# Kernel tuning notes

Measured on AMD Instinct MI355X. Metric: run time of the kernel, lower is better.

## Reference

```python
import jax, jax.numpy as jnp
import numpy as np

Q_STEPS, Q_TOKENS = 16, 64
KV_STEPS, KV_TOKENS = 64, 64
WINDOW = 2
TOPK = 32
DIM = 512
BATCH = 8
NUM_CONTEXTS = 2


def build_local_mask(q_steps, q_tokens, kv_steps, kv_tokens, window):
    # centers: nearest kv step for each query step
    centers = np.round(np.linspace(0, kv_steps - 1, q_steps)).astype(np.int64)
    steps = np.arange(kv_steps)
    allowed = np.abs(steps[None, :] - centers[:, None]) <= window  # [q_steps, kv_steps]
    allowed = np.repeat(np.repeat(allowed, q_tokens, axis=0), kv_tokens, axis=1)
    return jnp.where(jnp.asarray(allowed), 0.0, -jnp.inf).astype(jnp.float32)


MASK = build_local_mask(Q_STEPS, Q_TOKENS, KV_STEPS, KV_TOKENS, WINDOW)


def setup_inputs() -> dict:
    key = jax.random.key(0)
    ks = jax.random.split(key, 12)
    s = 1.0 / np.sqrt(DIM)
    return {
        "query": jax.random.normal(ks[0], (BATCH, Q_STEPS, Q_TOKENS, DIM), jnp.float32),
        "source": jax.random.normal(ks[1], (BATCH, KV_STEPS, KV_TOKENS, DIM), jnp.float32),
        "ctx1": jax.random.normal(ks[2], (BATCH, DIM), jnp.float32),
        "ctx2": jax.random.normal(ks[3], (BATCH, DIM), jnp.float32),
        "Wq": jax.random.normal(ks[4], (DIM, DIM), jnp.float32) * s,
        "bq": jnp.zeros((DIM,), jnp.float32),
        "Wk": jax.random.normal(ks[5], (DIM, DIM), jnp.float32) * s,
        "bk": jnp.zeros((DIM,), jnp.float32),
        "Wv": jax.random.normal(ks[6], (DIM, DIM), jnp.float32) * s,
        "bv": jnp.zeros((DIM,), jnp.float32),
        "Wo": jax.random.normal(ks[7], (DIM, DIM), jnp.float32) * s,
        "bo": jnp.zeros((DIM,), jnp.float32),
        "Wc": jax.random.normal(ks[8], (NUM_CONTEXTS * DIM, 2 * DIM), jnp.float32) * s,
        "bc": jnp.zeros((2 * DIM,), jnp.float32),
    }


def reference(query, source, ctx1, ctx2, Wq, bq, Wk, bk, Wv, bv, Wo, bo, Wc, bc):
    B = query.shape[0]
    # CrossScaleCondition: fuse contexts -> per-batch FiLM params gamma, beta [B, dim]
    fused = jnp.concatenate([ctx1, ctx2], axis=-1)          # [B, num_contexts*dim]
    gb = fused @ Wc + bc                                     # [B, 2*dim]
    gamma, beta = jnp.split(gb, 2, axis=-1)

    q_flat = query.reshape(B, Q_STEPS * Q_TOKENS, DIM)       # [B, Lq, d]
    src_flat = source.reshape(B, KV_STEPS * KV_TOKENS, DIM)  # [B, Lkv, d]

    q_mod = q_flat * (1.0 + gamma[:, None, :]) + beta[:, None, :]
    q = q_mod @ Wq + bq
    k = src_flat @ Wk + bk
    v = src_flat @ Wv + bv

    scores = jnp.einsum('bqd,bkd->bqk', q, k) / jnp.sqrt(jnp.float32(DIM))
    scores = scores + MASK[None]                             # local window mask

    topk_scores, topk_idx = jax.lax.top_k(scores, TOPK)      # [B, Lq, k]
    selected_v = jax.vmap(lambda vb, ib: vb[ib])(v, topk_idx)  # [B, Lq, k, d]

    attn = jax.nn.softmax(topk_scores, axis=-1)
    out = jnp.einsum('bqk,bqkd->bqd', attn, selected_v)
    out = out @ Wo + bo
    return out.reshape(B, Q_STEPS, Q_TOKENS, DIM)
```

## Files before the change

kernel.cpp:

```cpp
#include <hip/hip_runtime.h>

#define NWIN 320
#define SCORE_SCALE 0.04419417382415922f

__constant__ int CENTERS[16] = {0,4,8,13,17,21,25,29,34,38,42,46,50,55,59,63};

typedef __attribute__((ext_vector_type(8))) short v8s;
typedef __attribute__((ext_vector_type(4))) float v4f;

__device__ __forceinline__ float bflo(unsigned u) { return __uint_as_float(u << 16); }
__device__ __forceinline__ float bfhi(unsigned u) { return __uint_as_float(u & 0xffff0000u); }
__device__ __forceinline__ float bf2f(unsigned short h) { return __uint_as_float(((unsigned)h) << 16); }
__device__ __forceinline__ unsigned short f2bf(float x) {
  unsigned u = __float_as_uint(x);
  unsigned r = 0x7fffu + ((u >> 16) & 1u);
  return (unsigned short)((u + r) >> 16);
}

__device__ __forceinline__ int t64_off(int r, int k) {
  return ((r & 31) << 7) + (((((r >> 5) << 2) | (k >> 3)) ^ (r & 7)) << 4) + ((k & 7) << 1);
}
__device__ __forceinline__ int frag_off(int r, int g) {
  return ((r & 31) << 7) + (((((r >> 5) << 2) | g) ^ (r & 7)) << 4);
}

__device__ __forceinline__ void gload_lds16(const void* g, void* l) {
  __builtin_amdgcn_global_load_lds((const __attribute__((address_space(1))) unsigned int*)g,
                                   (__attribute__((address_space(3))) unsigned int*)l, 16, 0, 0);
}

__device__ __forceinline__ void cvt8pair(float4 a, float4 b, uint4& hi4, uint4& lo4) {
  float v[8] = {a.x, a.y, a.z, a.w, b.x, b.y, b.z, b.w};
  unsigned short h[8], l[8];
  #pragma unroll
  for (int e = 0; e < 8; ++e) {
    h[e] = f2bf(v[e]);
    l[e] = f2bf(v[e] - bf2f(h[e]));
  }
  hi4.x = (unsigned)h[0] | ((unsigned)h[1] << 16);
  hi4.y = (unsigned)h[2] | ((unsigned)h[3] << 16);
  hi4.z = (unsigned)h[4] | ((unsigned)h[5] << 16);
  hi4.w = (unsigned)h[6] | ((unsigned)h[7] << 16);
  lo4.x = (unsigned)l[0] | ((unsigned)l[1] << 16);
  lo4.y = (unsigned)l[2] | ((unsigned)l[3] << 16);
  lo4.z = (unsigned)l[4] | ((unsigned)l[5] << 16);
  lo4.w = (unsigned)l[6] | ((unsigned)l[7] << 16);
}

__device__ __forceinline__ uint4 cvt8hi(float4 a, float4 b) {
  uint4 r;
  r.x = (unsigned)f2bf(a.x) | ((unsigned)f2bf(a.y) << 16);
  r.y = (unsigned)f2bf(a.z) | ((unsigned)f2bf(a.w) << 16);
  r.z = (unsigned)f2bf(b.x) | ((unsigned)f2bf(b.y) << 16);
  r.w = (unsigned)f2bf(b.z) | ((unsigned)f2bf(b.w) << 16);
  return r;
}

__device__ __forceinline__ uint2 cvt4(float4 a) {
  uint2 r;
  r.x = (unsigned)f2bf(a.x) | ((unsigned)f2bf(a.y) << 16);
  r.y = (unsigned)f2bf(a.z) | ((unsigned)f2bf(a.w) << 16);
  return r;
}

__global__ void film_part(const float* __restrict__ ctx1, const float* __restrict__ ctx2,
                          const float* __restrict__ Wc, float* __restrict__ part)
{
  const int b = blockIdx.y, sl = blockIdx.x, j = threadIdx.x;
  const int i0 = sl * 128;
  float acc = 0.f;
  #pragma unroll 4
  for (int t = 0; t < 128; ++t) {
    const int i = i0 + t;
    const float f = (i < 512) ? ctx1[b * 512 + i] : ctx2[b * 512 + i - 512];
    acc = fmaf(f, Wc[(size_t)i * 1024 + j], acc);
  }
  part[(b * 8 + sl) * 1024 + j] = acc;
}

__global__ void film_reduce(const float* __restrict__ part, const float* __restrict__ bc,
                            float* __restrict__ gb)
{
  const int b = blockIdx.x, j = threadIdx.x;
  float acc = bc[j];
  #pragma unroll
  for (int sl = 0; sl < 8; ++sl) acc += part[(b * 8 + sl) * 1024 + j];
  gb[b * 1024 + j] = acc;
}

__global__ void u_kernel(const float* __restrict__ Wk, const float* __restrict__ bq,
                         float* __restrict__ u)
{
  const int d = blockIdx.x, lane = threadIdx.x;
  float4 a0 = *(const float4*)&Wk[(size_t)d * 512 + lane * 8];
  float4 a1 = *(const float4*)&Wk[(size_t)d * 512 + lane * 8 + 4];
  float4 c0 = *(const float4*)&bq[lane * 8];
  float4 c1 = *(const float4*)&bq[lane * 8 + 4];
  float s = a0.x*c0.x + a0.y*c0.y + a0.z*c0.z + a0.w*c0.w
          + a1.x*c1.x + a1.y*c1.y + a1.z*c1.z + a1.w*c1.w;
  #pragma unroll
  for (int off = 32; off > 0; off >>= 1) s += __shfl_xor(s, off, 64);
  if (lane == 0) u[d] = s * SCORE_SCALE;
}

__global__ __launch_bounds__(256) void wsplit_kernel(
    const float* __restrict__ Wq, const float* __restrict__ Wk,
    unsigned short* __restrict__ Wqh, unsigned short* __restrict__ Wql,
    unsigned short* __restrict__ Wkh, unsigned short* __restrict__ Wkl)
{
  const int b = blockIdx.x;
  const int mat = b >> 7;
  const float* Wsrc = mat ? Wk : Wq;
  unsigned short* Wh = mat ? Wkh : Wqh;
  unsigned short* Wl = mat ? Wkl : Wql;
  const size_t e0 = (((size_t)(b & 127) * 256) + threadIdx.x) * 8;
  float4 x0 = *(const float4*)&Wsrc[e0];
  float4 x1 = *(const float4*)&Wsrc[e0 + 4];
  uint4 h4, l4;
  cvt8pair(x0, x1, h4, l4);
  *(uint4*)&Wh[e0] = h4;
  *(uint4*)&Wl[e0] = l4;
}

__global__ __launch_bounds__(256) void gmat_mfma(
    const unsigned short* __restrict__ Wqh, const unsigned short* __restrict__ Wql,
    const unsigned short* __restrict__ Wkh, const unsigned short* __restrict__ Wkl,
    unsigned short* __restrict__ Gt)
{
  const int tid  = threadIdx.x;
  const int lane = tid & 63, l15 = lane & 15, g = lane >> 4;
  const int wave = tid >> 6;
  const int t  = ((int)blockIdx.x << 2) | wave;
  const int ti = t >> 5, tj = t & 31;
  const int ib = ti << 4, jb = tj << 4;
  const size_t arow = (size_t)(ib + l15) * 512 + (g << 3);
  const size_t brow = (size_t)(jb + l15) * 512 + (g << 3);

  v4f acc = (v4f){0.f, 0.f, 0.f, 0.f};
  #pragma unroll 4
  for (int kk = 0; kk < 16; ++kk) {
    const int kd = kk * 32;
    const v8s ah = *(const v8s*)&Wqh[arow + kd];
    const v8s al = *(const v8s*)&Wql[arow + kd];
    const v8s bh = *(const v8s*)&Wkh[brow + kd];
    const v8s bl = *(const v8s*)&Wkl[brow + kd];
    acc = __builtin_amdgcn_mfma_f32_16x16x32_bf16(ah, bh, acc, 0, 0, 0);
    acc = __builtin_amdgcn_mfma_f32_16x16x32_bf16(al, bh, acc, 0, 0, 0);
    acc = __builtin_amdgcn_mfma_f32_16x16x32_bf16(ah, bl, acc, 0, 0, 0);
  }

  #pragma unroll
  for (int k = 0; k < 4; ++k) {
    const int gi = ib + (g << 2) + k;
    const int gj = jb + l15;
    const float v = acc[k] * SCORE_SCALE;
    const unsigned short hi = f2bf(v);
    const unsigned short lo = f2bf(v - bf2f(hi));
    const int toff = t64_off(gj & 63, gi & 31);
    *(unsigned short*)((char*)Gt + ((size_t)((gi >> 5) * 8 + (gj >> 6)) << 12) + toff) = hi;
    *(unsigned short*)((char*)Gt + ((size_t)(((gi >> 5) + 16) * 8 + (gj >> 6)) << 12) + toff) = lo;
  }
}

__global__ __launch_bounds__(256) void wconv_kernel(
    const float* __restrict__ Wv, const float* __restrict__ Wo,
    unsigned short* __restrict__ Wvt, unsigned short* __restrict__ Wot)
{
  __shared__ char img[32768];
  const int ktile = blockIdx.x;
  const int mat   = blockIdx.y;
  const float* W = mat ? Wo : Wv;
  unsigned short* Dt = mat ? Wot : Wvt;
  const int tid = threadIdx.x;
  const int k  = tid >> 3;
  const int nt = tid & 7;
  #pragma unroll
  for (int e4 = 0; e4 < 16; ++e4) {
    float4 w = *(const float4*)&W[(size_t)(ktile * 32 + k) * 512 + nt * 64 + e4 * 4];
    float vv[4] = {w.x, w.y, w.z, w.w};
    #pragma unroll
    for (int c = 0; c < 4; ++c) {
      const int n = e4 * 4 + c;
      *(unsigned short*)(img + nt * 4096 + t64_off(n, k)) = f2bf(vv[c]);
    }
  }
  __syncthreads();
  const uint4* src = (const uint4*)img;
  uint4* dst = (uint4*)((char*)Dt + (size_t)ktile * 32768);
  for (int i = tid; i < 2048; i += 256) dst[i] = src[i];
}

__global__ __launch_bounds__(256) void proj_split(
    const float* __restrict__ A, const unsigned short* __restrict__ Bt,
    const float* __restrict__ bias, const float* __restrict__ gb,
    unsigned short* __restrict__ Qgt)
{
  __shared__ char smem[24576];
  char* const LAh = smem;
  char* const LAl = smem + 4096;
  char* const LBh = smem + 8192;
  char* const LBl = smem + 16384;

  const int tid  = threadIdx.x;
  const int lane = tid & 63, l15 = lane & 15, g = lane >> 4;
  const int wave = tid >> 6, wm = wave >> 1, wn = wave & 1;
  const int bid = blockIdx.x;
  const int xcd = bid & 7, idx = bid >> 3;
  const int mBlk = (idx & 15) | (xcd << 4);
  const int nBlk = idx >> 4;

  const int sr = tid >> 2;
  const int sq = tid & 3;
  const size_t arow = (size_t)(mBlk * 64 + sr) * 512 + sq * 8;
  const int gbbase = ((mBlk >> 4) * 1024) + sq * 8;
  const int awoff = t64_off(sr, sq * 8);

  int aoff[2], boff[4];
  #pragma unroll
  for (int fm = 0; fm < 2; ++fm) aoff[fm] = frag_off(wm * 32 + fm * 16 + l15, g);
  #pragma unroll
  for (int fn = 0; fn < 4; ++fn) {
    const int n = wn * 64 + fn * 16 + l15;
    boff[fn] = ((n >> 6) << 12) + frag_off(n & 63, g);
  }

  v4f acc[2][4];
  #pragma unroll
  for (int fm = 0; fm < 2; ++fm)
    #pragma unroll
    for (int fn = 0; fn < 4; ++fn) acc[fm][fn] = (v4f){0.f, 0.f, 0.f, 0.f};

  for (int tk = 0; tk < 16; ++tk) {
    const int kd = tk * 32;
    {
      const char* gsh = (const char*)Bt + ((size_t)(tk * 8 + nBlk * 2) << 12) + (size_t)tid * 16;
      const char* gsl = (const char*)Bt + ((size_t)((tk + 16) * 8 + nBlk * 2) << 12) + (size_t)tid * 16;
      #pragma unroll
      for (int i = 0; i < 2; ++i) {
        gload_lds16(gsh + i * 4096, LBh + (wave << 10) + i * 4096);
        gload_lds16(gsl + i * 4096, LBl + (wave << 10) + i * 4096);
      }
    }
    {
      float4 x0 = *(const float4*)&A[arow + kd];
      float4 x1 = *(const float4*)&A[arow + kd + 4];
      float4 g0 = *(const float4*)&gb[gbbase + kd];
      float4 g1 = *(const float4*)&gb[gbbase + kd + 4];
      float4 b0 = *(const float4*)&gb[gbbase + 512 + kd];
      float4 b1 = *(const float4*)&gb[gbbase + 512 + kd + 4];
      x0.x = fmaf(x0.x, 1.f + g0.x, b0.x); x0.y = fmaf(x0.y, 1.f + g0.y, b0.y);
      x0.z = fmaf(x0.z, 1.f + g0.z, b0.z); x0.w = fmaf(x0.w, 1.f + g0.w, b0.w);
      x1.x = fmaf(x1.x, 1.f + g1.x, b1.x); x1.y = fmaf(x1.y, 1.f + g1.y, b1.y);
      x1.z = fmaf(x1.z, 1.f + g1.z, b1.z); x1.w = fmaf(x1.w, 1.f + g1.w, b1.w);
      uint4 hi4, lo4;
      cvt8pair(x0, x1, hi4, lo4);
      *(uint4*)(LAh + awoff) = hi4;
      *(uint4*)(LAl + awoff) = lo4;
    }
    __syncthreads();
    const v8s ah0 = *(const v8s*)(LAh + aoff[0]);
    const v8s ah1 = *(const v8s*)(LAh + aoff[1]);
    const v8s al0 = *(const v8s*)(LAl + aoff[0]);
    const v8s al1 = *(const v8s*)(LAl + aoff[1]);
    #pragma unroll
    for (int fn = 0; fn < 4; ++fn) {
      const v8s bh = *(const v8s*)(LBh + boff[fn]);
      const v8s bl = *(const v8s*)(LBl + boff[fn]);
      acc[0][fn] = __builtin_amdgcn_mfma_f32_16x16x32_bf16(ah0, bh, acc[0][fn], 0, 0, 0);
      acc[1][fn] = __builtin_amdgcn_mfma_f32_16x16x32_bf16(ah1, bh, acc[1][fn], 0, 0, 0);
      acc[0][fn] = __builtin_amdgcn_mfma_f32_16x16x32_bf16(al0, bh, acc[0][fn], 0, 0, 0);
      acc[1][fn] = __builtin_amdgcn_mfma_f32_16x16x32_bf16(al1, bh, acc[1][fn], 0, 0, 0);
      acc[0][fn] = __builtin_amdgcn_mfma_f32_16x16x32_bf16(ah0, bl, acc[0][fn], 0, 0, 0);
      acc[1][fn] = __builtin_amdgcn_mfma_f32_16x16x32_bf16(ah1, bl, acc[1][fn], 0, 0, 0);
    }
    __syncthreads();
  }

  #pragma unroll
  for (int fn = 0; fn < 4; ++fn) {
    const int col = nBlk * 128 + wn * 64 + fn * 16 + l15;
    const float bv = bias[col];
    const int kt = col >> 5;
    const int kk = col & 31;
    #pragma unroll
    for (int fm = 0; fm < 2; ++fm) {
      const int r0 = wm * 32 + fm * 16 + g * 4;
      #pragma unroll
      for (int k = 0; k < 4; ++k) {
        const float vv = acc[fm][fn][k] + bv;
        const unsigned short hi = f2bf(vv);
        const unsigned short lo = f2bf(vv - bf2f(hi));
        const int toff = t64_off(r0 + k, kk);
        *(unsigned short*)((char*)Qgt + ((size_t)(kt * 128 + mBlk) << 12) + toff) = hi;
        *(unsigned short*)((char*)Qgt + ((size_t)((kt + 16) * 128 + mBlk) << 12) + toff) = lo;
      }
    }
  }
}

__global__ __launch_bounds__(512) void proj_v(
    const float* __restrict__ A, const unsigned short* __restrict__ Bt,
    const float* __restrict__ bias, unsigned short* __restrict__ Cb)
{
  __shared__ char smem[4096 + 32768];
  char* const LA = smem;
  char* const LB = smem + 4096;

  const int tid  = threadIdx.x;
  const int lane = tid & 63, l15 = lane & 15, g = lane >> 4;
  const int wave = tid >> 6, wm = wave >> 2, wn = wave & 3;
  const int mBlk = blockIdx.x;

  const int sr  = tid >> 3;
  const int sq4 = tid & 7;
  const size_t arow = (size_t)(mBlk * 64 + sr) * 512 + sq4 * 4;
  const int awoff = t64_off(sr, sq4 * 4);

  int aoff[2], boff[8];
  #pragma unroll
  for (int fm = 0; fm < 2; ++fm) aoff[fm] = frag_off(wm * 32 + fm * 16 + l15, g);
  #pragma unroll
  for (int fn = 0; fn < 8; ++fn) {
    const int n = wn * 128 + fn * 16 + l15;
    boff[fn] = ((n >> 6) << 12) + frag_off(n & 63, g);
  }

  v4f acc[2][8];
  #pragma unroll
  for (int fm = 0; fm < 2; ++fm)
    #pragma unroll
    for (int fn = 0; fn < 8; ++fn) acc[fm][fn] = (v4f){0.f, 0.f, 0.f, 0.f};

  for (int tk = 0; tk < 16; ++tk) {
    const int kd = tk * 32;
    {
      const char* gs = (const char*)Bt + ((size_t)tk << 15) + (wave << 12) + (lane << 4);
      char* ld = LB + (wave << 12);
      #pragma unroll
      for (int i = 0; i < 4; ++i) gload_lds16(gs + (i << 10), ld + (i << 10));
    }
    {
      float4 x = *(const float4*)&A[arow + kd];
      *(uint2*)(LA + awoff) = cvt4(x);
    }
    __syncthreads();
    const v8s a0 = *(const v8s*)(LA + aoff[0]);
    const v8s a1 = *(const v8s*)(LA + aoff[1]);
    #pragma unroll
    for (int fn = 0; fn < 8; ++fn) {
      const v8s bb = *(const v8s*)(LB + boff[fn]);
      acc[0][fn] = __builtin_amdgcn_mfma_f32_16x16x32_bf16(a0, bb, acc[0][fn], 0, 0, 0);
      acc[1][fn] = __builtin_amdgcn_mfma_f32_16x16x32_bf16(a1, bb, acc[1][fn], 0, 0, 0);
    }
    __syncthreads();
  }

  #pragma unroll
  for (int fn = 0; fn < 8; ++fn) {
    const int col = wn * 128 + fn * 16 + l15;
    const float bv = bias[col];
    #pragma unroll
    for (int fm = 0; fm < 2; ++fm) {
      const int r0 = mBlk * 64 + wm * 32 + fm * 16 + g * 4;
      #pragma unroll
      for (int k = 0; k < 4; ++k)
        Cb[(size_t)(r0 + k) * 512 + col] = f2bf(acc[fm][fn][k] + bv);
    }
  }
}

__global__ __launch_bounds__(256) void proj_o(
    const float* __restrict__ A, const unsigned short* __restrict__ Bt,
    const float* __restrict__ bias, float* __restrict__ Cf)
{
  __shared__ char smem[12288];
  char* const LA = smem;
  char* const LB = smem + 4096;

  const int tid  = threadIdx.x;
  const int lane = tid & 63, l15 = lane & 15, g = lane >> 4;
  const int wave = tid >> 6, wm = wave >> 1, wn = wave & 1;
  const int bid = blockIdx.x;
  const int xcd = bid & 7, idx = bid >> 3;
  const int mBlk = (idx & 15) | (xcd << 4);
  const int nBlk = idx >> 4;

  const int sr = tid >> 2;
  const int sq = tid & 3;
  const size_t arow = (size_t)(mBlk * 64 + sr) * 512 + sq * 8;
  const int awoff = t64_off(sr, sq * 8);

  int aoff[2], boff[4];
  #pragma unroll
  for (int fm = 0; fm < 2; ++fm) aoff[fm] = frag_off(wm * 32 + fm * 16 + l15, g);
  #pragma unroll
  for (int fn = 0; fn < 4; ++fn) {
    const int n = wn * 64 + fn * 16 + l15;
    boff[fn] = ((n >> 6) << 12) + frag_off(n & 63, g);
  }

  v4f acc[2][4];
  #pragma unroll
  for (int fm = 0; fm < 2; ++fm)
    #pragma unroll
    for (int fn = 0; fn < 4; ++fn) acc[fm][fn] = (v4f){0.f, 0.f, 0.f, 0.f};

  for (int tk = 0; tk < 16; ++tk) {
    const int kd = tk * 32;
    {
      const char* gs = (const char*)Bt + ((size_t)tk << 15) + ((size_t)nBlk << 13) + (size_t)tid * 16;
      #pragma unroll
      for (int i = 0; i < 2; ++i)
        gload_lds16(gs + i * 4096, LB + (wave << 10) + i * 4096);
    }
    {
      float4 x0 = *(const float4*)&A[arow + kd];
      float4 x1 = *(const float4*)&A[arow + kd + 4];
      *(uint4*)(LA + awoff) = cvt8hi(x0, x1);
    }
    __syncthreads();
    const v8s a0 = *(const v8s*)(LA + aoff[0]);
    const v8s a1 = *(const v8s*)(LA + aoff[1]);
    #pragma unroll
    for (int fn = 0; fn < 4; ++fn) {
      const v8s bb = *(const v8s*)(LB + boff[fn]);
      acc[0][fn] = __builtin_amdgcn_mfma_f32_16x16x32_bf16(a0, bb, acc[0][fn], 0, 0, 0);
      acc[1][fn] = __builtin_amdgcn_mfma_f32_16x16x32_bf16(a1, bb, acc[1][fn], 0, 0, 0);
    }
    __syncthreads();
  }

  #pragma unroll
  for (int fn = 0; fn < 4; ++fn) {
    const int col = nBlk * 128 + wn * 64 + fn * 16 + l15;
    const float bv = bias[col];
    #pragma unroll
    for (int fm = 0; fm < 2; ++fm) {
      const int r0 = mBlk * 64 + wm * 32 + fm * 16 + g * 4;
      #pragma unroll
      for (int k = 0; k < 4; ++k)
        Cf[(size_t)(r0 + k) * 512 + col] = acc[fm][fn][k] + bv;
    }
  }
}

__global__ __launch_bounds__(256) void scores_mfma(
    const unsigned short* __restrict__ Qgt, const float* __restrict__ SRC,
    float* __restrict__ S)
{
  const int bs = blockIdx.y;
  const int s = bs & 15, b = bs >> 4;
  const int c  = CENTERS[s];
  const int lo = (c - 2 > 0) ? c - 2 : 0;
  const int hi = (c + 2 < 63) ? c + 2 : 63;
  if ((int)blockIdx.x > hi - lo) return;

  __shared__ char smem[16384];
  char* const LAh = smem;
  char* const LAl = smem + 4096;
  char* const LBh = smem + 8192;
  char* const LBl = smem + 12288;

  const int tid = threadIdx.x;
  const int lane = tid & 63, l15 = lane & 15, g = lane >> 4;
  const int wave = tid >> 6, wm = wave >> 1, wn = wave & 1;
  const int kvrow0 = (b << 12) + ((lo + (int)blockIdx.x) << 6);
  const int qbase  = bs << 6;
  const int sr = tid >> 2, sq = tid & 3;
  const size_t krow = (size_t)(kvrow0 + sr) * 512 + sq * 8;
  const int awoff = t64_off(sr, sq * 8);

  int aoff[2], boff[2];
  #pragma unroll
  for (int f = 0; f < 2; ++f) {
    aoff[f] = frag_off(wm * 32 + f * 16 + l15, g);
    boff[f] = frag_off(wn * 32 + f * 16 + l15, g);
  }

  v4f acc[2][2];
  #pragma unroll
  for (int i = 0; i < 2; ++i)
    #pragma unroll
    for (int j = 0; j < 2; ++j) acc[i][j] = (v4f){0.f, 0.f, 0.f, 0.f};

  for (int tk = 0; tk < 16; ++tk) {
    const int kd = tk * 32;
    {
      const char* gah = (const char*)Qgt + ((size_t)(tk * 128 + bs) << 12) + (size_t)tid * 16;
      const char* gal = (const char*)Qgt + ((size_t)((tk + 16) * 128 + bs) << 12) + (size_t)tid * 16;
      gload_lds16(gah, LAh + (wave << 10));
      gload_lds16(gal, LAl + (wave << 10));
    }
    {
      float4 y0 = *(const float4*)&SRC[krow + kd];
      float4 y1 = *(const float4*)&SRC[krow + kd + 4];
      uint4 bhi, blo;
      cvt8pair(y0, y1, bhi, blo);
      *(uint4*)(LBh + awoff) = bhi;
      *(uint4*)(LBl + awoff) = blo;
    }
    __syncthreads();
    const v8s a0h = *(const v8s*)(LAh + aoff[0]);
    const v8s a1h = *(const v8s*)(LAh + aoff[1]);
    const v8s a0l = *(const v8s*)(LAl + aoff[0]);
    const v8s a1l = *(const v8s*)(LAl + aoff[1]);
    const v8s b0h = *(const v8s*)(LBh + boff[0]);
    const v8s b1h = *(const v8s*)(LBh + boff[1]);
    const v8s b0l = *(const v8s*)(LBl + boff[0]);
    const v8s b1l = *(const v8s*)(LBl + boff[1]);
    acc[0][0] = __builtin_amdgcn_mfma_f32_16x16x32_bf16(a0h, b0h, acc[0][0], 0, 0, 0);
    acc[0][1] = __builtin_amdgcn_mfma_f32_16x16x32_bf16(a0h, b1h, acc[0][1], 0, 0, 0);
    acc[1][0] = __builtin_amdgcn_mfma_f32_16x16x32_bf16(a1h, b0h, acc[1][0], 0, 0, 0);
    acc[1][1] = __builtin_amdgcn_mfma_f32_16x16x32_bf16(a1h, b1h, acc[1][1], 0, 0, 0);
    acc[0][0] = __builtin_amdgcn_mfma_f32_16x16x32_bf16(a0l, b0h, acc[0][0], 0, 0, 0);
    acc[0][1] = __builtin_amdgcn_mfma_f32_16x16x32_bf16(a0l, b1h, acc[0][1], 0, 0, 0);
    acc[1][0] = __builtin_amdgcn_mfma_f32_16x16x32_bf16(a1l, b0h, acc[1][0], 0, 0, 0);
    acc[1][1] = __builtin_amdgcn_mfma_f32_16x16x32_bf16(a1l, b1h, acc[1][1], 0, 0, 0);
    acc[0][0] = __builtin_amdgcn_mfma_f32_16x16x32_bf16(a0h, b0l, acc[0][0], 0, 0, 0);
    acc[0][1] = __builtin_amdgcn_mfma_f32_16x16x32_bf16(a0h, b1l, acc[0][1], 0, 0, 0);
    acc[1][0] = __builtin_amdgcn_mfma_f32_16x16x32_bf16(a1h, b0l, acc[1][0], 0, 0, 0);
    acc[1][1] = __builtin_amdgcn_mfma_f32_16x16x32_bf16(a1h, b1l, acc[1][1], 0, 0, 0);
    __syncthreads();
  }

  #pragma unroll
  for (int fn = 0; fn < 2; ++fn) {
    const int cl = wn * 32 + fn * 16 + l15;
    const int colS = ((int)blockIdx.x << 6) + cl;
    #pragma unroll
    for (int fm = 0; fm < 2; ++fm) {
      const int r0 = qbase + wm * 32 + fm * 16 + g * 4;
      #pragma unroll
      for (int k = 0; k < 4; ++k)
        S[(size_t)(r0 + k) * NWIN + colS] = acc[fm][fn][k];
    }
  }
}

__global__ __launch_bounds__(256) void topk_pv(
    const float* __restrict__ S, const unsigned short* __restrict__ Vb,
    float* __restrict__ O)
{
  __shared__ int   sel_i[4][32];
  __shared__ float sel_p[4][32];

  const int lane = threadIdx.x & 63;
  const int wv   = threadIdx.x >> 6;
  const int b0   = blockIdx.x;
  const int grp  = (b0 & 7) + ((b0 >> 7) << 3);
  const int blk  = (b0 >> 3) & 15;
  const int row  = (((grp << 4) + blk) << 2) + wv;
  const int b    = row >> 10;
  const int s    = (row >> 6) & 15;
  const int c    = CENTERS[s];
  const int lo   = (c - 2 > 0) ? c - 2 : 0;
  const int hi   = (c + 2 < 63) ? c + 2 : 63;
  const int L    = (hi - lo + 1) << 6;
  const size_t vbase = ((size_t)b << 12) + ((size_t)lo << 6);

  const float* srow = S + (size_t)row * NWIN;
  float f[5]; unsigned uo[5];
  #pragma unroll
  for (int j = 0; j < 5; ++j) {
    const int idx = lane + (j << 6);
    const float v = (idx < L) ? srow[idx] : -__builtin_inff();
    f[j] = v;
    const unsigned fb = __float_as_uint(v);
    uo[j] = (fb & 0x80000000u) ? ~fb : (fb | 0x80000000u);
  }

  float m = f[0];
  #pragma unroll
  for (int j = 1; j < 5; ++j) m = fmaxf(m, f[j]);
  #pragma unroll
  for (int off = 32; off > 0; off >>= 1) m = fmaxf(m, __shfl_xor(m, off, 64));

  unsigned T = 0u;
  for (int bit = 31; bit >= 0; --bit) {
    const unsigned cand = T | (1u << bit);
    int cnt = 0;
    #pragma unroll
    for (int j = 0; j < 5; ++j)
      cnt += __popcll(__ballot(uo[j] >= cand));
    if (cnt >= 32) T = cand;
  }

  int base = 0;
  #pragma unroll
  for (int j = 0; j < 5; ++j) {
    const unsigned long long gm = __ballot(uo[j] > T);
    if (uo[j] > T) {
      const int rank = base + __builtin_amdgcn_mbcnt_hi(
          (unsigned)(gm >> 32), __builtin_amdgcn_mbcnt_lo((unsigned)gm, 0));
      sel_i[wv][rank] = lane + (j << 6);
      sel_p[wv][rank] = __expf(f[j] - m);
    }
    base += __popcll(gm);
  }
  #pragma unroll
  for (int j = 0; j < 5; ++j) {
    const unsigned long long em = __ballot(uo[j] == T);
    if (uo[j] == T) {
      const int er = base + __builtin_amdgcn_mbcnt_hi(
          (unsigned)(em >> 32), __builtin_amdgcn_mbcnt_lo((unsigned)em, 0));
      if (er < 32) {
        sel_i[wv][er] = lane + (j << 6);
        sel_p[wv][er] = __expf(f[j] - m);
      }
    }
    base += __popcll(em);
  }

  asm volatile("s_waitcnt lgkmcnt(0)" ::: "memory");

  const int   si = sel_i[wv][lane & 31];
  const float sp = sel_p[wv][lane & 31];
  float dp = (lane < 32) ? sp : 0.f;
  #pragma unroll
  for (int off = 32; off > 0; off >>= 1) dp += __shfl_xor(dp, off, 64);

  float oacc[8] = {0.f,0.f,0.f,0.f,0.f,0.f,0.f,0.f};
  #pragma unroll
  for (int t = 0; t < 32; ++t) {
    const int   idx_t = __builtin_amdgcn_readlane(si, t);
    const float p_t   = __uint_as_float(
        (unsigned)__builtin_amdgcn_readlane((int)__float_as_uint(sp), t));
    const unsigned short* vrow = Vb + ((vbase + (size_t)idx_t) << 9);
    #pragma unroll
    for (int e = 0; e < 4; ++e) {
      const unsigned raw = *(const unsigned*)&vrow[(lane << 1) + (e << 7)];
      oacc[2*e]     = fmaf(p_t, bflo(raw), oacc[2*e]);
      oacc[2*e + 1] = fmaf(p_t, bfhi(raw), oacc[2*e + 1]);
    }
  }

  const float inv = 1.0f / dp;
  float* orow = O + ((size_t)row << 9);
  #pragma unroll
  for (int e = 0; e < 4; ++e) {
    float2 o2 = make_float2(oacc[2*e] * inv, oacc[2*e + 1] * inv);
    *(float2*)&orow[(lane << 1) + (e << 7)] = o2;
  }
}

extern "C" void kernel_launch(void* const* d_in, const int* in_sizes, int n_in,
                              void* d_out, int out_size, void* d_ws, size_t ws_size,
                              hipStream_t stream)
{
  (void)in_sizes; (void)n_in; (void)out_size; (void)ws_size;

  const float* query  = (const float*)d_in[0];
  const float* source = (const float*)d_in[1];
  const float* ctx1   = (const float*)d_in[2];
  const float* ctx2   = (const float*)d_in[3];
  const float* Wq     = (const float*)d_in[4];
  const float* bq     = (const float*)d_in[5];
  const float* Wk     = (const float*)d_in[6];
  const float* Wv     = (const float*)d_in[8];
  const float* bv     = (const float*)d_in[9];
  const float* Wo     = (const float*)d_in[10];
  const float* bo     = (const float*)d_in[11];
  const float* Wc     = (const float*)d_in[12];
  const float* bc     = (const float*)d_in[13];
  float* out = (float*)d_out;

  char* ws = (char*)d_ws;
  unsigned short* Qgt  = (unsigned short*)(ws);
  unsigned short* v    = (unsigned short*)(ws + 16777216);
  float*          S    = (float*)(ws + 50331648);
  float*          ctx  = (float*)(ws + 60817408);
  unsigned short* Gt   = (unsigned short*)(ws + 77594624);
  unsigned short* Wvt  = (unsigned short*)(ws + 78643200);
  unsigned short* Wot  = (unsigned short*)(ws + 79167488);
  float*          gb   = (float*)(ws + 79691776);
  float*          part = (float*)(ws + 79724544);
  float*          u    = (float*)(ws + 79986688);
  unsigned short* Wqh  = (unsigned short*)(ws + 79988736);
  unsigned short* Wql  = (unsigned short*)(ws + 80513024);
  unsigned short* Wkh  = (unsigned short*)(ws + 81037312);
  unsigned short* Wkl  = (unsigned short*)(ws + 81561600);

  film_part   <<<dim3(8, 8), 1024, 0, stream>>>(ctx1, ctx2, Wc, part);
  film_reduce <<<8, 1024, 0, stream>>>(part, bc, gb);
  u_kernel    <<<512, 64, 0, stream>>>(Wk, bq, u);
  wsplit_kernel<<<256, 256, 0, stream>>>(Wq, Wk, Wqh, Wql, Wkh, Wkl);
  gmat_mfma   <<<256, 256, 0, stream>>>(Wqh, Wql, Wkh, Wkl, Gt);
  wconv_kernel<<<dim3(16, 2), 256, 0, stream>>>(Wv, Wo, Wvt, Wot);

  proj_split<<<512, 256, 0, stream>>>(query, Gt, u, gb, Qgt);
  proj_v<<<512, 512, 0, stream>>>(source, Wvt, bv, v);
  scores_mfma<<<dim3(5, 128), 256, 0, stream>>>(Qgt, source, S);
  topk_pv<<<2048, 256, 0, stream>>>(S, v, ctx);
  proj_o<<<512, 256, 0, stream>>>(ctx, Wot, bo, out);
}
```

Measured before the change: 152.5 us.

## Merge prep and projection kernels into combined multi-role launches

Combines six small weight-preparation and FiLM kernels into two launches that pick their role from the block index. The Q-split and V projections now run in one 1536-block launch, interleaved by block index modulo 3. The V projection is retiled to 256-thread blocks covering half the output columns. The aim is to cut launch overhead and let independent projections share the GPU at the same time, at the cost of branch-divergent kernels and different register and occupancy behaviour.

```diff
diff --git a/kernel.cpp b/kernel.cpp
--- a/kernel.cpp
+++ b/kernel.cpp
@@ -56,315 +56,311 @@
   return r;
 }
 
-__device__ __forceinline__ uint2 cvt4(float4 a) {
-  uint2 r;
-  r.x = (unsigned)f2bf(a.x) | ((unsigned)f2bf(a.y) << 16);
-  r.y = (unsigned)f2bf(a.z) | ((unsigned)f2bf(a.w) << 16);
-  return r;
-}
-
-__global__ void film_part(const float* __restrict__ ctx1, const float* __restrict__ ctx2,
-                          const float* __restrict__ Wc, float* __restrict__ part)
-{
-  const int b = blockIdx.y, sl = blockIdx.x, j = threadIdx.x;
-  const int i0 = sl * 128;
-  float acc = 0.f;
-  #pragma unroll 4
-  for (int t = 0; t < 128; ++t) {
-    const int i = i0 + t;
-    const float f = (i < 512) ? ctx1[b * 512 + i] : ctx2[b * 512 + i - 512];
-    acc = fmaf(f, Wc[(size_t)i * 1024 + j], acc);
-  }
-  part[(b * 8 + sl) * 1024 + j] = acc;
-}
-
-__global__ void film_reduce(const float* __restrict__ part, const float* __restrict__ bc,
-                            float* __restrict__ gb)
-{
-  const int b = blockIdx.x, j = threadIdx.x;
-  float acc = bc[j];
-  #pragma unroll
-  for (int sl = 0; sl < 8; ++sl) acc += part[(b * 8 + sl) * 1024 + j];
-  gb[b * 1024 + j] = acc;
-}
-
-__global__ void u_kernel(const float* __restrict__ Wk, const float* __restrict__ bq,
-                         float* __restrict__ u)
-{
-  const int d = blockIdx.x, lane = threadIdx.x;
-  float4 a0 = *(const float4*)&Wk[(size_t)d * 512 + lane * 8];
-  float4 a1 = *(const float4*)&Wk[(size_t)d * 512 + lane * 8 + 4];
-  float4 c0 = *(const float4*)&bq[lane * 8];
-  float4 c1 = *(const float4*)&bq[lane * 8 + 4];
-  float s = a0.x*c0.x + a0.y*c0.y + a0.z*c0.z + a0.w*c0.w
-          + a1.x*c1.x + a1.y*c1.y + a1.z*c1.z + a1.w*c1.w;
-  #pragma unroll
-  for (int off = 32; off > 0; off >>= 1) s += __shfl_xor(s, off, 64);
-  if (lane == 0) u[d] = s * SCORE_SCALE;
-}
-
-__global__ __launch_bounds__(256) void wsplit_kernel(
-    const float* __restrict__ Wq, const float* __restrict__ Wk,
+__global__ __launch_bounds__(256) void prep1_kernel(
+    const float* __restrict__ ctx1, const float* __restrict__ ctx2,
+    const float* __restrict__ Wc,  float* __restrict__ part,
+    const float* __restrict__ Wk,  const float* __restrict__ bq, float* __restrict__ u,
+    const float* __restrict__ Wq,
     unsigned short* __restrict__ Wqh, unsigned short* __restrict__ Wql,
-    unsigned short* __restrict__ Wkh, unsigned short* __restrict__ Wkl)
-{
-  const int b = blockIdx.x;
-  const int mat = b >> 7;
-  const float* Wsrc = mat ? Wk : Wq;
-  unsigned short* Wh = mat ? Wkh : Wqh;
-  unsigned short* Wl = mat ? Wkl : Wql;
-  const size_t e0 = (((size_t)(b & 127) * 256) + threadIdx.x) * 8;
-  float4 x0 = *(const float4*)&Wsrc[e0];
-  float4 x1 = *(const float4*)&Wsrc[e0 + 4];
-  uint4 h4, l4;
-  cvt8pair(x0, x1, h4, l4);
-  *(uint4*)&Wh[e0] = h4;
-  *(uint4*)&Wl[e0] = l4;
-}
-
-__global__ __launch_bounds__(256) void gmat_mfma(
-    const unsigned short* __restrict__ Wqh, const unsigned short* __restrict__ Wql,
-    const unsigned short* __restrict__ Wkh, const unsigned short* __restrict__ Wkl,
-    unsigned short* __restrict__ Gt)
-{
-  const int tid  = threadIdx.x;
-  const int lane = tid & 63, l15 = lane & 15, g = lane >> 4;
-  const int wave = tid >> 6;
-  const int t  = ((int)blockIdx.x << 2) | wave;
-  const int ti = t >> 5, tj = t & 31;
-  const int ib = ti << 4, jb = tj << 4;
-  const size_t arow = (size_t)(ib + l15) * 512 + (g << 3);
-  const size_t brow = (size_t)(jb + l15) * 512 + (g << 3);
-
-  v4f acc = (v4f){0.f, 0.f, 0.f, 0.f};
-  #pragma unroll 4
-  for (int kk = 0; kk < 16; ++kk) {
-    const int kd = kk * 32;
-    const v8s ah = *(const v8s*)&Wqh[arow + kd];
-    const v8s al = *(const v8s*)&Wql[arow + kd];
-    const v8s bh = *(const v8s*)&Wkh[brow + kd];
-    const v8s bl = *(const v8s*)&Wkl[brow + kd];
-    acc = __builtin_amdgcn_mfma_f32_16x16x32_bf16(ah, bh, acc, 0, 0, 0);
-    acc = __builtin_amdgcn_mfma_f32_16x16x32_bf16(al, bh, acc, 0, 0, 0);
-    acc = __builtin_amdgcn_mfma_f32_16x16x32_bf16(ah, bl, acc, 0, 0, 0);
-  }
-
-  #pragma unroll
-  for (int k = 0; k < 4; ++k) {
-    const int gi = ib + (g << 2) + k;
-    const int gj = jb + l15;
-    const float v = acc[k] * SCORE_SCALE;
-    const unsigned short hi = f2bf(v);
-    const unsigned short lo = f2bf(v - bf2f(hi));
-    const int toff = t64_off(gj & 63, gi & 31);
-    *(unsigned short*)((char*)Gt + ((size_t)((gi >> 5) * 8 + (gj >> 6)) << 12) + toff) = hi;
-    *(unsigned short*)((char*)Gt + ((size_t)(((gi >> 5) + 16) * 8 + (gj >> 6)) << 12) + toff) = lo;
-  }
-}
-
-__global__ __launch_bounds__(256) void wconv_kernel(
+    unsigned short* __restrict__ Wkh, unsigned short* __restrict__ Wkl,
     const float* __restrict__ Wv, const float* __restrict__ Wo,
     unsigned short* __restrict__ Wvt, unsigned short* __restrict__ Wot)
 {
   __shared__ char img[32768];
-  const int ktile = blockIdx.x;
-  const int mat   = blockIdx.y;
-  const float* W = mat ? Wo : Wv;
-  unsigned short* Dt = mat ? Wot : Wvt;
+  const int bid = blockIdx.x;
   const int tid = threadIdx.x;
-  const int k  = tid >> 3;
-  const int nt = tid & 7;
-  #pragma unroll
-  for (int e4 = 0; e4 < 16; ++e4) {
-    float4 w = *(const float4*)&W[(size_t)(ktile * 32 + k) * 512 + nt * 64 + e4 * 4];
-    float vv[4] = {w.x, w.y, w.z, w.w};
-    #pragma unroll
-    for (int c = 0; c < 4; ++c) {
-      const int n = e4 * 4 + c;
-      *(unsigned short*)(img + nt * 4096 + t64_off(n, k)) = f2bf(vv[c]);
-    }
-  }
-  __syncthreads();
-  const uint4* src = (const uint4*)img;
-  uint4* dst = (uint4*)((char*)Dt + (size_t)ktile * 32768);
-  for (int i = tid; i < 2048; i += 256) dst[i] = src[i];
-}
-
-__global__ __launch_bounds__(256) void proj_split(
-    const float* __restrict__ A, const unsigned short* __restrict__ Bt,
-    const float* __restrict__ bias, const float* __restrict__ gb,
-    unsigned short* __restrict__ Qgt)
+
+  if (bid < 256) {
+    const int b = bid >> 5, sl = (bid >> 2) & 7, jq = bid & 3;
+    const int j = jq * 256 + tid;
+    const int i0 = sl * 128;
+    float acc = 0.f;
+    #pragma unroll 4
+    for (int t = 0; t < 128; ++t) {
+      const int i = i0 + t;
+      const float f = (i < 512) ? ctx1[b * 512 + i] : ctx2[b * 512 + i - 512];
+      acc = fmaf(f, Wc[(size_t)i * 1024 + j], acc);
+    }
+    part[(b * 8 + sl) * 1024 + j] = acc;
+  } else if (bid < 384) {
+    const int d = (bid - 256) * 4 + (tid >> 6);
+    const int lane = tid & 63;
+    float4 a0 = *(const float4*)&Wk[(size_t)d * 512 + lane * 8];
+    float4 a1 = *(const float4*)&Wk[(size_t)d * 512 + lane * 8 + 4];
+    float4 c0 = *(const float4*)&bq[lane * 8];
+    float4 c1 = *(const float4*)&bq[lane * 8 + 4];
+    float s = a0.x*c0.x + a0.y*c0.y + a0.z*c0.z + a0.w*c0.w
+            + a1.x*c1.x + a1.y*c1.y + a1.z*c1.z + a1.w*c1.w;
+    #pragma unroll
+    for (int off = 32; off > 0; off >>= 1) s += __shfl_xor(s, off, 64);
+    if (lane == 0) u[d] = s * SCORE_SCALE;
+  } else if (bid < 640) {
+    const int b = bid - 384;
+    const int mat = b >> 7;
+    const float* Wsrc = mat ? Wk : Wq;
+    unsigned short* Wh = mat ? Wkh : Wqh;
+    unsigned short* Wl = mat ? Wkl : Wql;
+    const size_t e0 = (((size_t)(b & 127) * 256) + tid) * 8;
+    float4 x0 = *(const float4*)&Wsrc[e0];
+    float4 x1 = *(const float4*)&Wsrc[e0 + 4];
+    uint4 h4, l4;
+    cvt8pair(x0, x1, h4, l4);
+    *(uint4*)&Wh[e0] = h4;
+    *(uint4*)&Wl[e0] = l4;
+  } else {
+    const int cb = bid - 640;
+    const int ktile = cb & 15;
+    const int mat   = cb >> 4;
+    const float* W = mat ? Wo : Wv;
+    unsigned short* Dt = mat ? Wot : Wvt;
+    const int k  = tid >> 3;
+    const int nt = tid & 7;
+    #pragma unroll
+    for (int e4 = 0; e4 < 16; ++e4) {
+      float4 w = *(const float4*)&W[(size_t)(ktile * 32 + k) * 512 + nt * 64 + e4 * 4];
+      float vv[4] = {w.x, w.y, w.z, w.w};
+      #pragma unroll
+      for (int c = 0; c < 4; ++c) {
+        const int n = e4 * 4 + c;
+        *(unsigned short*)(img + nt * 4096 + t64_off(n, k)) = f2bf(vv[c]);
+      }
+    }
+    __syncthreads();
+    const uint4* src = (const uint4*)img;
+    uint4* dst = (uint4*)((char*)Dt + (size_t)ktile * 32768);
+    for (int i = tid; i < 2048; i += 256) dst[i] = src[i];
+  }
+}
+
+__global__ __launch_bounds__(256) void prep2_kernel(
+    const unsigned short* __restrict__ Wqh, const unsigned short* __restrict__ Wql,
+    const unsigned short* __restrict__ Wkh, const unsigned short* __restrict__ Wkl,
+    unsigned short* __restrict__ Gt,
+    const float* __restrict__ part, const float* __restrict__ bc,
+    float* __restrict__ gb)
+{
+  const int bid = blockIdx.x;
+  const int tid = threadIdx.x;
+
+  if (bid < 256) {
+    const int lane = tid & 63, l15 = lane & 15, g = lane >> 4;
+    const int wave = tid >> 6;
+    const int t  = (bid << 2) | wave;
+    const int ti = t >> 5, tj = t & 31;
+    const int ib = ti << 4, jb = tj << 4;
+    const size_t arow = (size_t)(ib + l15) * 512 + (g << 3);
+    const size_t brow = (size_t)(jb + l15) * 512 + (g << 3);
+
+    v4f acc = (v4f){0.f, 0.f, 0.f, 0.f};
+    #pragma unroll 4
+    for (int kk = 0; kk < 16; ++kk) {
+      const int kd = kk * 32;
+      const v8s ah = *(const v8s*)&Wqh[arow + kd];
+      const v8s al = *(const v8s*)&Wql[arow + kd];
+      const v8s bh = *(const v8s*)&Wkh[brow + kd];
+      const v8s bl = *(const v8s*)&Wkl[brow + kd];
+      acc = __builtin_amdgcn_mfma_f32_16x16x32_bf16(ah, bh, acc, 0, 0, 0);
+      acc = __builtin_amdgcn_mfma_f32_16x16x32_bf16(al, bh, acc, 0, 0, 0);
+      acc = __builtin_amdgcn_mfma_f32_16x16x32_bf16(ah, bl, acc, 0, 0, 0);
+    }
+    #pragma unroll
+    for (int k = 0; k < 4; ++k) {
+      const int gi = ib + (g << 2) + k;
+      const int gj = jb + l15;
+      const float v = acc[k] * SCORE_SCALE;
+      const unsigned short hi = f2bf(v);
+      const unsigned short lo = f2bf(v - bf2f(hi));
+      const int toff = t64_off(gj & 63, gi & 31);
+      *(unsigned short*)((char*)Gt + ((size_t)((gi >> 5) * 8 + (gj >> 6)) << 12) + toff) = hi;
+      *(unsigned short*)((char*)Gt + ((size_t)(((gi >> 5) + 16) * 8 + (gj >> 6)) << 12) + toff) = lo;
+    }
+  } else {
+    const int rb = bid - 256;
+    const int b = rb >> 2, jq = rb & 3;
+    const int j = jq * 256 + tid;
+    float acc = bc[j];
+    #pragma unroll
+    for (int sl = 0; sl < 8; ++sl) acc += part[(b * 8 + sl) * 1024 + j];
+    gb[b * 1024 + j] = acc;
+  }
+}
+
+__global__ __launch_bounds__(256) void mega_kernel(
+    const float* __restrict__ query, const unsigned short* __restrict__ Gt,
+    const float* __restrict__ ubias, const float* __restrict__ gb,
+    unsigned short* __restrict__ Qgt,
+    const float* __restrict__ source, const unsigned short* __restrict__ Wvt,
+    const float* __restrict__ bv, unsigned short* __restrict__ Vb)
 {
   __shared__ char smem[24576];
-  char* const LAh = smem;
-  char* const LAl = smem + 4096;
-  char* const LBh = smem + 8192;
-  char* const LBl = smem + 16384;
-
-  const int tid  = threadIdx.x;
+  const int bid = blockIdx.x;
+  const int tid = threadIdx.x;
   const int lane = tid & 63, l15 = lane & 15, g = lane >> 4;
   const int wave = tid >> 6, wm = wave >> 1, wn = wave & 1;
-  const int bid = blockIdx.x;
-  const int xcd = bid & 7, idx = bid >> 3;
-  const int mBlk = (idx & 15) | (xcd << 4);
-  const int nBlk = idx >> 4;
-
-  const int sr = tid >> 2;
-  const int sq = tid & 3;
-  const size_t arow = (size_t)(mBlk * 64 + sr) * 512 + sq * 8;
-  const int gbbase = ((mBlk >> 4) * 1024) + sq * 8;
-  const int awoff = t64_off(sr, sq * 8);
-
-  int aoff[2], boff[4];
-  #pragma unroll
-  for (int fm = 0; fm < 2; ++fm) aoff[fm] = frag_off(wm * 32 + fm * 16 + l15, g);
-  #pragma unroll
-  for (int fn = 0; fn < 4; ++fn) {
-    const int n = wn * 64 + fn * 16 + l15;
-    boff[fn] = ((n >> 6) << 12) + frag_off(n & 63, g);
-  }
-
-  v4f acc[2][4];
-  #pragma unroll
-  for (int fm = 0; fm < 2; ++fm)
-    #pragma unroll
-    for (int fn = 0; fn < 4; ++fn) acc[fm][fn] = (v4f){0.f, 0.f, 0.f, 0.f};
-
-  for (int tk = 0; tk < 16; ++tk) {
-    const int kd = tk * 32;
-    {
-      const char* gsh = (const char*)Bt + ((size_t)(tk * 8 + nBlk * 2) << 12) + (size_t)tid * 16;
-      const char* gsl = (const char*)Bt + ((size_t)((tk + 16) * 8 + nBlk * 2) << 12) + (size_t)tid * 16;
-      #pragma unroll
-      for (int i = 0; i < 2; ++i) {
-        gload_lds16(gsh + i * 4096, LBh + (wave << 10) + i * 4096);
-        gload_lds16(gsl + i * 4096, LBl + (wave << 10) + i * 4096);
-      }
-    }
-    {
-      float4 x0 = *(const float4*)&A[arow + kd];
-      float4 x1 = *(const float4*)&A[arow + kd + 4];
-      float4 g0 = *(const float4*)&gb[gbbase + kd];
-      float4 g1 = *(const float4*)&gb[gbbase + kd + 4];
-      float4 b0 = *(const float4*)&gb[gbbase + 512 + kd];
-      float4 b1 = *(const float4*)&gb[gbbase + 512 + kd + 4];
-      x0.x = fmaf(x0.x, 1.f + g0.x, b0.x); x0.y = fmaf(x0.y, 1.f + g0.y, b0.y);
-      x0.z = fmaf(x0.z, 1.f + g0.z, b0.z); x0.w = fmaf(x0.w, 1.f + g0.w, b0.w);
-      x1.x = fmaf(x1.x, 1.f + g1.x, b1.x); x1.y = fmaf(x1.y, 1.f + g1.y, b1.y);
-      x1.z = fmaf(x1.z, 1.f + g1.z, b1.z); x1.w = fmaf(x1.w, 1.f + g1.w, b1.w);
-      uint4 hi4, lo4;
-      cvt8pair(x0, x1, hi4, lo4);
-      *(uint4*)(LAh + awoff) = hi4;
-      *(uint4*)(LAl + awoff) = lo4;
-    }
-    __syncthreads();
-    const v8s ah0 = *(const v8s*)(LAh + aoff[0]);
-    const v8s ah1 = *(const v8s*)(LAh + aoff[1]);
-    const v8s al0 = *(const v8s*)(LAl + aoff[0]);
-    const v8s al1 = *(const v8s*)(LAl + aoff[1]);
+  const int r3 = bid % 3, q3 = bid / 3;
+
+  if (r3 == 2) {
+    char* const LAh = smem;
+    char* const LAl = smem + 4096;
+    char* const LBh = smem + 8192;
+    char* const LBl = smem + 16384;
+
+    const int sb = q3;
+    const int xcd = sb & 7, idx = sb >> 3;
+    const int mBlk = (idx & 15) | (xcd << 4);
+    const int nBlk = idx >> 4;
+
+    const int sr = tid >> 2;
+    const int sq = tid & 3;
+    const size_t arow = (size_t)(mBlk * 64 + sr) * 512 + sq * 8;
+    const int gbbase = ((mBlk >> 4) * 1024) + sq * 8;
+    const int awoff = t64_off(sr, sq * 8);
+
+    int aoff[2], boff[4];
+    #pragma unroll
+    for (int fm = 0; fm < 2; ++fm) aoff[fm] = frag_off(wm * 32 + fm * 16 + l15, g);
     #pragma unroll
     for (int fn = 0; fn < 4; ++fn) {
-      const v8s bh = *(const v8s*)(LBh + boff[fn]);
-      const v8s bl = *(const v8s*)(LBl + boff[fn]);
-      acc[0][fn] = __builtin_amdgcn_mfma_f32_16x16x32_bf16(ah0, bh, acc[0][fn], 0, 0, 0);
-      acc[1][fn] = __builtin_amdgcn_mfma_f32_16x16x32_bf16(ah1, bh, acc[1][fn], 0, 0, 0);
-      acc[0][fn] = __builtin_amdgcn_mfma_f32_16x16x32_bf16(al0, bh, acc[0][fn], 0, 0, 0);
-      acc[1][fn] = __builtin_amdgcn_mfma_f32_16x16x32_bf16(al1, bh, acc[1][fn], 0, 0, 0);
-      acc[0][fn] = __builtin_amdgcn_mfma_f32_16x16x32_bf16(ah0, bl, acc[0][fn], 0, 0, 0);
-      acc[1][fn] = __builtin_amdgcn_mfma_f32_16x16x32_bf16(ah1, bl, acc[1][fn], 0, 0, 0);
-    }
-    __syncthreads();
-  }
-
-  #pragma unroll
-  for (int fn = 0; fn < 4; ++fn) {
-    const int col = nBlk * 128 + wn * 64 + fn * 16 + l15;
-    const float bv = bias[col];
-    const int kt = col >> 5;
-    const int kk = col & 31;
-    #pragma unroll
-    for (int fm = 0; fm < 2; ++fm) {
-      const int r0 = wm * 32 + fm * 16 + g * 4;
-      #pragma unroll
-      for (int k = 0; k < 4; ++k) {
-        const float vv = acc[fm][fn][k] + bv;
-        const unsigned short hi = f2bf(vv);
-        const unsigned short lo = f2bf(vv - bf2f(hi));
-        const int toff = t64_off(r0 + k, kk);
-        *(unsigned short*)((char*)Qgt + ((size_t)(kt * 128 + mBlk) << 12) + toff) = hi;
-        *(unsigned short*)((char*)Qgt + ((size_t)((kt + 16) * 128 + mBlk) << 12) + toff) = lo;
-      }
-    }
-  }
-}
-
-__global__ __launch_bounds__(512) void proj_v(
-    const float* __restrict__ A, const unsigned short* __restrict__ Bt,
-    const float* __restrict__ bias, unsigned short* __restrict__ Cb)
-{
-  __shared__ char smem[4096 + 32768];
-  char* const LA = smem;
-  char* const LB = smem + 4096;
-
-  const int tid  = threadIdx.x;
-  const int lane = tid & 63, l15 = lane & 15, g = lane >> 4;
-  const int wave = tid >> 6, wm = wave >> 2, wn = wave & 3;
-  const int mBlk = blockIdx.x;
-
-  const int sr  = tid >> 3;
-  const int sq4 = tid & 7;
-  const size_t arow = (size_t)(mBlk * 64 + sr) * 512 + sq4 * 4;
-  const int awoff = t64_off(sr, sq4 * 4);
-
-  int aoff[2], boff[8];
-  #pragma unroll
-  for (int fm = 0; fm < 2; ++fm) aoff[fm] = frag_off(wm * 32 + fm * 16 + l15, g);
-  #pragma unroll
-  for (int fn = 0; fn < 8; ++fn) {
-    const int n = wn * 128 + fn * 16 + l15;
-    boff[fn] = ((n >> 6) << 12) + frag_off(n & 63, g);
-  }
-
-  v4f acc[2][8];
-  #pragma unroll
-  for (int fm = 0; fm < 2; ++fm)
-    #pragma unroll
-    for (int fn = 0; fn < 8; ++fn) acc[fm][fn] = (v4f){0.f, 0.f, 0.f, 0.f};
-
-  for (int tk = 0; tk < 16; ++tk) {
-    const int kd = tk * 32;
-    {
-      const char* gs = (const char*)Bt + ((size_t)tk << 15) + (wave << 12) + (lane << 4);
-      char* ld = LB + (wave << 12);
-      #pragma unroll
-      for (int i = 0; i < 4; ++i) gload_lds16(gs + (i << 10), ld + (i << 10));
-    }
-    {
-      float4 x = *(const float4*)&A[arow + kd];
-      *(uint2*)(LA + awoff) = cvt4(x);
-    }
-    __syncthreads();
-    const v8s a0 = *(const v8s*)(LA + aoff[0]);
-    const v8s a1 = *(const v8s*)(LA + aoff[1]);
+      const int n = wn * 64 + fn * 16 + l15;
+      boff[fn] = ((n >> 6) << 12) + frag_off(n & 63, g);
+    }
+
+    v4f acc[2][4];
+    #pragma unroll
+    for (int fm = 0; fm < 2; ++fm)
+      #pragma unroll
+      for (int fn = 0; fn < 4; ++fn) acc[fm][fn] = (v4f){0.f, 0.f, 0.f, 0.f};
+
+    for (int tk = 0; tk < 16; ++tk) {
+      const int kd = tk * 32;
+      {
+        const char* gsh = (const char*)Gt + ((size_t)(tk * 8 + nBlk * 2) << 12) + (size_t)tid * 16;
+        const char* gsl = (const char*)Gt + ((size_t)((tk + 16) * 8 + nBlk * 2) << 12) + (size_t)tid * 16;
+        #pragma unroll
+        for (int i = 0; i < 2; ++i) {
+          gload_lds16(gsh + i * 4096, LBh + (wave << 10) + i * 4096);
+          gload_lds16(gsl + i * 4096, LBl + (wave << 10) + i * 4096);
+        }
+      }
+      {
+        float4 x0 = *(const float4*)&query[arow + kd];
+        float4 x1 = *(const float4*)&query[arow + kd + 4];
+        float4 g0 = *(const float4*)&gb[gbbase + kd];
+        float4 g1 = *(const float4*)&gb[gbbase + kd + 4];
+        float4 b0 = *(const float4*)&gb[gbbase + 512 + kd];
+        float4 b1 = *(const float4*)&gb[gbbase + 512 + kd + 4];
+        x0.x = fmaf(x0.x, 1.f + g0.x, b0.x); x0.y = fmaf(x0.y, 1.f + g0.y, b0.y);
+        x0.z = fmaf(x0.z, 1.f + g0.z, b0.z); x0.w = fmaf(x0.w, 1.f + g0.w, b0.w);
+        x1.x = fmaf(x1.x, 1.f + g1.x, b1.x); x1.y = fmaf(x1.y, 1.f + g1.y, b1.y);
+        x1.z = fmaf(x1.z, 1.f + g1.z, b1.z); x1.w = fmaf(x1.w, 1.f + g1.w, b1.w);
+        uint4 hi4, lo4;
+        cvt8pair(x0, x1, hi4, lo4);
+        *(uint4*)(LAh + awoff) = hi4;
+        *(uint4*)(LAl + awoff) = lo4;
+      }
+      __syncthreads();
+      const v8s ah0 = *(const v8s*)(LAh + aoff[0]);
+      const v8s ah1 = *(const v8s*)(LAh + aoff[1]);
+      const v8s al0 = *(const v8s*)(LAl + aoff[0]);
+      const v8s al1 = *(const v8s*)(LAl + aoff[1]);
+      #pragma unroll
+      for (int fn = 0; fn < 4; ++fn) {
+        const v8s bh = *(const v8s*)(LBh + boff[fn]);
+        const v8s bl = *(const v8s*)(LBl + boff[fn]);
+        acc[0][fn] = __builtin_amdgcn_mfma_f32_16x16x32_bf16(ah0, bh, acc[0][fn], 0, 0, 0);
+        acc[1][fn] = __builtin_amdgcn_mfma_f32_16x16x32_bf16(ah1, bh, acc[1][fn], 0, 0, 0);
+        acc[0][fn] = __builtin_amdgcn_mfma_f32_16x16x32_bf16(al0, bh, acc[0][fn], 0, 0, 0);
+        acc[1][fn] = __builtin_amdgcn_mfma_f32_16x16x32_bf16(al1, bh, acc[1][fn], 0, 0, 0);
+        acc[0][fn] = __builtin_amdgcn_mfma_f32_16x16x32_bf16(ah0, bl, acc[0][fn], 0, 0, 0);
+        acc[1][fn] = __builtin_amdgcn_mfma_f32_16x16x32_bf16(ah1, bl, acc[1][fn], 0, 0, 0);
+      }
+      __syncthreads();
+    }
+
+    #pragma unroll
+    for (int fn = 0; fn < 4; ++fn) {
+      const int col = nBlk * 128 + wn * 64 + fn * 16 + l15;
+      const float bvv = ubias[col];
+      const int kt = col >> 5;
+      const int kk = col & 31;
+      #pragma unroll
+      for (int fm = 0; fm < 2; ++fm) {
+        const int r0 = wm * 32 + fm * 16 + g * 4;
+        #pragma unroll
+        for (int k = 0; k < 4; ++k) {
+          const float vv = acc[fm][fn][k] + bvv;
+          const unsigned short hi = f2bf(vv);
+          const unsigned short lo = f2bf(vv - bf2f(hi));
+          const int toff = t64_off(r0 + k, kk);
+          *(unsigned short*)((char*)Qgt + ((size_t)(kt * 128 + mBlk) << 12) + toff) = hi;
+          *(unsigned short*)((char*)Qgt + ((size_t)((kt + 16) * 128 + mBlk) << 12) + toff) = lo;
+        }
+      }
+    }
+  } else {
+    char* const LA = smem;
+    char* const LB = smem + 4096;
+
+    const int vb = q3 * 2 + r3;
+    const int nBlk = vb & 1;
+    const int mBlk = vb >> 1;
+
+    const int sr = tid >> 2;
+    const int sq = tid & 3;
+    const size_t arow = (size_t)(mBlk * 64 + sr) * 512 + sq * 8;
+    const int awoff = t64_off(sr, sq * 8);
+
+    int aoff[2], boff[8];
+    #pragma unroll
+    for (int fm = 0; fm < 2; ++fm) aoff[fm] = frag_off(wm * 32 + fm * 16 + l15, g);
     #pragma unroll
     for (int fn = 0; fn < 8; ++fn) {
-      const v8s bb = *(const v8s*)(LB + boff[fn]);
-      acc[0][fn] = __builtin_amdgcn_mfma_f32_16x16x32_bf16(a0, bb, acc[0][fn], 0, 0, 0);
-      acc[1][fn] = __builtin_amdgcn_mfma_f32_16x16x32_bf16(a1, bb, acc[1][fn], 0, 0, 0);
-    }
-    __syncthreads();
-  }
-
-  #pragma unroll
-  for (int fn = 0; fn < 8; ++fn) {
-    const int col = wn * 128 + fn * 16 + l15;
-    const float bv = bias[col];
-    #pragma unroll
-    for (int fm = 0; fm < 2; ++fm) {
-      const int r0 = mBlk * 64 + wm * 32 + fm * 16 + g * 4;
-      #pragma unroll
-      for (int k = 0; k < 4; ++k)
-        Cb[(size_t)(r0 + k) * 512 + col] = f2bf(acc[fm][fn][k] + bv);
+      const int n = wn * 128 + fn * 16 + l15;
+      boff[fn] = ((n >> 6) << 12) + frag_off(n & 63, g);
+    }
+
+    v4f acc[2][8];
+    #pragma unroll
+    for (int fm = 0; fm < 2; ++fm)
+      #pragma unroll
+      for (int fn = 0; fn < 8; ++fn) acc[fm][fn] = (v4f){0.f, 0.f, 0.f, 0.f};
+
+    for (int tk = 0; tk < 16; ++tk) {
+      const int kd = tk * 32;
+      {
+        const char* gs = (const char*)Wvt + ((size_t)(tk * 8 + nBlk * 4) << 12) + (size_t)tid * 16;
+        char* ld = LB + (wave << 10);
+        #pragma unroll
+        for (int i = 0; i < 4; ++i) gload_lds16(gs + i * 4096, ld + i * 4096);
+      }
+      {
+        float4 x0 = *(const float4*)&source[arow + kd];
+        float4 x1 = *(const float4*)&source[arow + kd + 4];
+        *(uint4*)(LA + awoff) = cvt8hi(x0, x1);
+      }
+      __syncthreads();
+      const v8s a0 = *(const v8s*)(LA + aoff[0]);
+      const v8s a1 = *(const v8s*)(LA + aoff[1]);
+      #pragma unroll
+      for (int fn = 0; fn < 8; ++fn) {
+        const v8s bb = *(const v8s*)(LB + boff[fn]);
+        acc[0][fn] = __builtin_amdgcn_mfma_f32_16x16x32_bf16(a0, bb, acc[0][fn], 0, 0, 0);
+        acc[1][fn] = __builtin_amdgcn_mfma_f32_16x16x32_bf16(a1, bb, acc[1][fn], 0, 0, 0);
+      }
+      __syncthreads();
+    }
+
+    #pragma unroll
+    for (int fn = 0; fn < 8; ++fn) {
+      const int col = nBlk * 256 + wn * 128 + fn * 16 + l15;
+      const float bvv = bv[col];
+      #pragma unroll
+      for (int fm = 0; fm < 2; ++fm) {
+        const int r0 = mBlk * 64 + wm * 32 + fm * 16 + g * 4;
+        #pragma unroll
+        for (int k = 0; k < 4; ++k)
+          Vb[(size_t)(r0 + k) * 512 + col] = f2bf(acc[fm][fn][k] + bvv);
+      }
     }
   }
 }
@@ -680,15 +676,10 @@
   unsigned short* Wkh  = (unsigned short*)(ws + 81037312);
   unsigned short* Wkl  = (unsigned short*)(ws + 81561600);
 
-  film_part   <<<dim3(8, 8), 1024, 0, stream>>>(ctx1, ctx2, Wc, part);
-  film_reduce <<<8, 1024, 0, stream>>>(part, bc, gb);
-  u_kernel    <<<512, 64, 0, stream>>>(Wk, bq, u);
-  wsplit_kernel<<<256, 256, 0, stream>>>(Wq, Wk, Wqh, Wql, Wkh, Wkl);
-  gmat_mfma   <<<256, 256, 0, stream>>>(Wqh, Wql, Wkh, Wkl, Gt);
-  wconv_kernel<<<dim3(16, 2), 256, 0, stream>>>(Wv, Wo, Wvt, Wot);
-
-  proj_split<<<512, 256, 0, stream>>>(query, Gt, u, gb, Qgt);
-  proj_v<<<512, 512, 0, stream>>>(source, Wvt, bv, v);
+  prep1_kernel<<<672, 256, 0, stream>>>(ctx1, ctx2, Wc, part, Wk, bq, u, Wq,
+                                        Wqh, Wql, Wkh, Wkl, Wv, Wo, Wvt, Wot);
+  prep2_kernel<<<288, 256, 0, stream>>>(Wqh, Wql, Wkh, Wkl, Gt, part, bc, gb);
+  mega_kernel<<<1536, 256, 0, stream>>>(query, Gt, u, gb, Qgt, source, Wvt, bv, v);
   scores_mfma<<<dim3(5, 128), 256, 0, stream>>>(Qgt, source, S);
   topk_pv<<<2048, 256, 0, stream>>>(S, v, ctx);
   proj_o<<<512, 256, 0, stream>>>(ctx, Wot, bo, out);
```

Measured after the change: 157.0 us. 1.03x slower.
